# Kernel tuning notes

Hardware: AMD Instinct MI355X
Metric: run time of the kernel (lower is better)

## Reference

```python
import jax, jax.numpy as jnp
import numpy as np

NUM_HEADS = 16
NUM_KV_HEADS = 8
HEAD_DIM = 128
SCALE = 1.0 / np.sqrt(HEAD_DIM)  # 0.08838834764831845
SEQ_LENS = [1536, 512, 1024, 1024]  # ragged packed sequences, total T=4096


def setup_inputs() -> dict:
    key = jax.random.key(0)
    k1, k2, k3 = jax.random.split(key, 3)
    T = sum(SEQ_LENS)
    q = jax.random.normal(k1, (T, NUM_HEADS * HEAD_DIM), dtype=jnp.float32)
    k = jax.random.normal(k2, (T, NUM_KV_HEADS * HEAD_DIM), dtype=jnp.float32)
    v = jax.random.normal(k3, (T, NUM_KV_HEADS * HEAD_DIM), dtype=jnp.float32)
    # positions restart at 0 for each packed sequence; jumps mark boundaries
    positions = jnp.asarray(np.concatenate([np.arange(L) for L in SEQ_LENS]), dtype=jnp.int32)
    return {"q": q, "k": k, "v": v, "positions": positions}


def reference(q, k, v, positions):
    T = q.shape[0]
    G = NUM_HEADS // NUM_KV_HEADS  # GQA group size
    qh = q.reshape(T, NUM_KV_HEADS, G, HEAD_DIM)
    kh = k.reshape(T, NUM_KV_HEADS, HEAD_DIM)
    vh = v.reshape(T, NUM_KV_HEADS, HEAD_DIM)
    # segment ids from position jumps (positions[i] != positions[i-1] + 1)
    jump = jnp.concatenate([
        jnp.zeros((1,), jnp.int32),
        (positions[1:] != positions[:-1] + 1).astype(jnp.int32),
    ])
    seg = jnp.cumsum(jump)  # [T]
    idx = jnp.arange(T)
    # attend only within the same packed sequence, causally
    mask = (seg[:, None] == seg[None, :]) & (idx[:, None] >= idx[None, :])  # [T, T]
    # scores: [kv_head, group, T_q, T_k]
    scores = jnp.einsum('tkgd,skd->kgts', qh, kh) * jnp.float32(SCALE)
    scores = jnp.where(mask[None, None], scores, jnp.float32(-1e30))
    p = jax.nn.softmax(scores, axis=-1)
    o = jnp.einsum('kgts,skd->tkgd', p, vh)
    return o.reshape(T, NUM_HEADS * HEAD_DIM)
```

## Files before the change

kernel.cpp:

```cpp
#include <hip/hip_runtime.h>
#include <cstdint>
#include <cstddef>

#define NUM_KV   8
#define GQA      2
#define HD       128
#define QSTRIDE  2048
#define KSTRIDE  1024
#define SCALE_LOG2E 0.12751741032075463f

typedef float    f32x4  __attribute__((ext_vector_type(4)));
typedef float    f32x2  __attribute__((ext_vector_type(2)));
typedef float    f32x16 __attribute__((ext_vector_type(16)));
typedef unsigned u32x4  __attribute__((ext_vector_type(4)));
typedef __bf16   bf16x8 __attribute__((ext_vector_type(8)));
typedef __bf16   bf16x2 __attribute__((ext_vector_type(2)));
typedef int      i32x2  __attribute__((ext_vector_type(2)));

union U8 { unsigned short u[8]; unsigned d[4]; u32x4 q; bf16x8 v; };

__device__ __forceinline__ unsigned pkb(float x, float y) {
    f32x2 f = {x, y};
    bf16x2 b = __builtin_convertvector(f, bf16x2);
    union { bf16x2 b; unsigned u; } c; c.b = b;
    return c.u;
}

__device__ __forceinline__ void pl32swap(unsigned &a, unsigned &b) {
    i32x2 r = __builtin_amdgcn_permlane32_swap((int)a, (int)b, false, false);
    a = (unsigned)r[0];
    b = (unsigned)r[1];
}

__global__ __launch_bounds__(512)
void swizzle_kv(const float* __restrict__ kg, const float* __restrict__ vg,
                unsigned short* __restrict__ Kswz, unsigned short* __restrict__ Vswz,
                int T, int NT)
{
    const int tt = blockIdx.x, h = blockIdx.y;
    const int tid = threadIdx.x;
    const int f = tid >> 6, lane = tid & 63;
    const int col = lane & 31, hk = lane >> 5;

    if (blockIdx.z == 0) {
        const int row = min(tt * 32 + col, T - 1);
        const float* src = kg + (size_t)row * KSTRIDE + h * HD + f * 16 + hk * 8;
        f32x4 a = ((const f32x4*)src)[0];
        f32x4 b = ((const f32x4*)src)[1];
        u32x4 W;
        W[0] = pkb(a[0], a[1]); W[1] = pkb(a[2], a[3]);
        W[2] = pkb(b[0], b[1]); W[3] = pkb(b[2], b[3]);
        *(u32x4*)(Kswz + (((size_t)h * NT + tt) * 8 + f) * 512 + lane * 8) = W;
    } else {
        const int d  = (f >> 1) * 32 + col;
        const int r0 = tt * 32 + (f & 1) * 16 + hk * 8;
        float x[8];
#pragma unroll
        for (int j = 0; j < 8; ++j) {
            const int row = min(r0 + j, T - 1);
            x[j] = vg[(size_t)row * KSTRIDE + h * HD + d];
        }
        u32x4 W;
        W[0] = pkb(x[0], x[1]); W[1] = pkb(x[2], x[3]);
        W[2] = pkb(x[4], x[5]); W[3] = pkb(x[6], x[7]);
        *(u32x4*)(Vswz + (((size_t)h * NT + tt) * 8 + f) * 512 + lane * 8) = W;
    }
}

__global__ __launch_bounds__(128, 2)
void attn_kernel(const float* __restrict__ qg, const unsigned short* __restrict__ Kswz,
                 const unsigned short* __restrict__ Vswz, const int* __restrict__ pos,
                 float* __restrict__ out, int T, int NT)
{
    __shared__ __align__(16) float Xb[64 * 64 + 32];
    __shared__ int Db[256];
    __shared__ int Sq[256];

    const int tid  = threadIdx.x;
    const int w    = tid >> 6;
    const int lane = tid & 63;
    const int col  = lane & 31;
    const int hk   = lane >> 5;

    const int bid = blockIdx.x;
    const int kvh = bid & 7;
    const int g   = (bid >> 3) & 1;
    const int qtr = bid >> 4;
    const int nq  = (T + 31) >> 5;

    for (int t = tid; t < nq; t += 128) {
        const int r0  = t * 32;
        const int tlo = (r0 - pos[r0]) >> 5;
        const int thi = (min(r0 + 32, T) + 31) >> 5;
        Db[t] = thi - tlo;
    }
    __syncthreads();
    for (int t = tid; t < nq; t += 128) {
        const int dt = Db[t];
        int rk = 0;
        for (int j = 0; j < nq; ++j) {
            const int dj = Db[j];
            rk += (dj > dt) || (dj == dt && j < t);
        }
        Sq[rk] = t;
    }
    __syncthreads();

    const int qt   = Sq[qtr];
    const int row0 = qt * 32;
    const int hq   = kvh * GQA + g;

    const int kend = min(row0 + 32, T);
    const int k_lo = row0 - pos[row0];

    const int qrow   = min(row0 + col, T - 1);
    const int rstart = qrow - pos[qrow];
    int rs_max = rstart;
    rs_max = max(rs_max, __shfl_xor(rs_max, 1));
    rs_max = max(rs_max, __shfl_xor(rs_max, 2));
    rs_max = max(rs_max, __shfl_xor(rs_max, 4));
    rs_max = max(rs_max, __shfl_xor(rs_max, 8));
    rs_max = max(rs_max, __shfl_xor(rs_max, 16));

    bf16x8 qf[8];
    {
        const float* qp = qg + (size_t)qrow * QSTRIDE + hq * HD + hk * 8;
#pragma unroll
        for (int c = 0; c < 8; ++c) {
            f32x4 f0 = ((const f32x4*)(qp + c * 16))[0];
            f32x4 f1 = ((const f32x4*)(qp + c * 16))[1];
            U8 u;
            u.d[0] = pkb(f0[0] * SCALE_LOG2E, f0[1] * SCALE_LOG2E);
            u.d[1] = pkb(f0[2] * SCALE_LOG2E, f0[3] * SCALE_LOG2E);
            u.d[2] = pkb(f1[0] * SCALE_LOG2E, f1[1] * SCALE_LOG2E);
            u.d[3] = pkb(f1[2] * SCALE_LOG2E, f1[3] * SCALE_LOG2E);
            qf[c] = u.v;
        }
    }

    f32x16 acc[4];
#pragma unroll
    for (int nt = 0; nt < 4; ++nt)
#pragma unroll
        for (int r = 0; r < 16; ++r) acc[nt][r] = 0.f;
    float l_lane = 0.f;

    const int t_lo = k_lo >> 5;
    const int t_hi = (kend + 31) >> 5;
    const unsigned short* kb_base = Kswz + (size_t)kvh * NT * 4096;
    const unsigned short* vb_base = Vswz + (size_t)kvh * NT * 4096;

    U8 kf[8], kfn[8], vf[8];
    int tt = t_lo + w;
    if (tt < t_hi) {
        const unsigned short* kp = kb_base + (size_t)tt * 4096 + lane * 8;
#pragma unroll
        for (int c = 0; c < 8; ++c) kf[c].q = *(const u32x4*)(kp + c * 512);
    }

    for (; tt < t_hi; tt += 2) {
        {
            const unsigned short* vp = vb_base + (size_t)tt * 4096 + lane * 8;
#pragma unroll
            for (int f = 0; f < 8; ++f) vf[f].q = *(const u32x4*)(vp + f * 512);
        }
        const int ttn = tt + 2;
        if (ttn < t_hi) {
            const unsigned short* kp = kb_base + (size_t)ttn * 4096 + lane * 8;
#pragma unroll
            for (int c = 0; c < 8; ++c) kfn[c].q = *(const u32x4*)(kp + c * 512);
        }

        f32x16 s;
#pragma unroll
        for (int r = 0; r < 16; ++r) s[r] = 0.f;
        __builtin_amdgcn_s_setprio(1);
#pragma unroll
        for (int c = 0; c < 8; ++c)
            s = __builtin_amdgcn_mfma_f32_32x32x16_bf16(kf[c].v, qf[c], s, 0, 0, 0);
        __builtin_amdgcn_s_setprio(0);

        const int kb = tt * 32;
        float p[16];
        if (kb >= rs_max && kb + 32 <= row0 + 1) {
#pragma unroll
            for (int r = 0; r < 16; ++r) { p[r] = exp2f(s[r]); l_lane += p[r]; }
        } else {
#pragma unroll
            for (int r = 0; r < 16; ++r) {
                const int key = kb + (r & 3) + 8 * (r >> 2) + 4 * hk;
                const float x = (key >= rstart && key <= qrow) ? s[r] : -3e38f;
                p[r] = exp2f(x);
                l_lane += p[r];
            }
        }

        unsigned a0 = pkb(p[0],  p[1]),  a1 = pkb(p[2],  p[3]);
        unsigned b0 = pkb(p[4],  p[5]),  b1 = pkb(p[6],  p[7]);
        pl32swap(a0, b0); pl32swap(a1, b1);
        unsigned c0 = pkb(p[8],  p[9]),  c1 = pkb(p[10], p[11]);
        unsigned d0 = pkb(p[12], p[13]), d1 = pkb(p[14], p[15]);
        pl32swap(c0, d0); pl32swap(c1, d1);
        U8 pa0, pa1;
        pa0.d[0] = a0; pa0.d[1] = a1; pa0.d[2] = b0; pa0.d[3] = b1;
        pa1.d[0] = c0; pa1.d[1] = c1; pa1.d[2] = d0; pa1.d[3] = d1;

        __builtin_amdgcn_s_setprio(1);
#pragma unroll
        for (int nt = 0; nt < 4; ++nt) {
            acc[nt] = __builtin_amdgcn_mfma_f32_32x32x16_bf16(pa0.v, vf[nt * 2].v,     acc[nt], 0, 0, 0);
            acc[nt] = __builtin_amdgcn_mfma_f32_32x32x16_bf16(pa1.v, vf[nt * 2 + 1].v, acc[nt], 0, 0, 0);
        }
        __builtin_amdgcn_s_setprio(0);

#pragma unroll
        for (int c = 0; c < 8; ++c) kf[c] = kfn[c];
    }

    const float lt = l_lane + __shfl_xor(l_lane, 32);

    if (w == 1) {
#pragma unroll
        for (int nt = 0; nt < 4; ++nt)
#pragma unroll
            for (int r = 0; r < 16; ++r)
                Xb[(nt * 16 + r) * 64 + lane] = acc[nt][r];
        if (hk == 0) Xb[4096 + col] = lt;
    }
    __syncthreads();
    if (w == 0) {
        const float ltot = lt + Xb[4096 + col];
#pragma unroll
        for (int nt = 0; nt < 4; ++nt)
#pragma unroll
            for (int r = 0; r < 16; ++r)
                acc[nt][r] += Xb[(nt * 16 + r) * 64 + lane];

#pragma unroll
        for (int r = 0; r < 16; ++r) {
            const int m  = (r & 3) + 8 * (r >> 2) + 4 * hk;
            const int rg = row0 + m;
            const float lm  = __shfl(ltot, m);
            const float inv = (lm > 0.f) ? (1.0f / lm) : 0.f;
            if (rg < T) {
                float* op = out + (size_t)rg * QSTRIDE + hq * HD + col;
#pragma unroll
                for (int nt = 0; nt < 4; ++nt)
                    op[nt * 32] = acc[nt][r] * inv;
            }
        }
    }
}

extern "C" void kernel_launch(void* const* d_in, const int* in_sizes, int n_in,
                              void* d_out, int out_size, void* d_ws, size_t ws_size,
                              hipStream_t stream) {
    const float* q   = (const float*)d_in[0];
    const float* k   = (const float*)d_in[1];
    const float* v   = (const float*)d_in[2];
    const int*   pos = (const int*)d_in[3];
    float* out = (float*)d_out;
    const int T  = in_sizes[0] / QSTRIDE;
    const int NT = (T + 31) / 32;

    unsigned short* Kswz = (unsigned short*)d_ws;
    unsigned short* Vswz = Kswz + (size_t)NUM_KV * NT * 4096;

    swizzle_kv<<<dim3(NT, NUM_KV, 2), 512, 0, stream>>>(k, v, Kswz, Vswz, T, NT);
    attn_kernel<<<dim3(NT * 16), 128, 0, stream>>>(q, Kswz, Vswz, pos, out, T, NT);
}
```

Before: 149.8 us.

## Split KV tiles across four waves per query tile with tree reduction

Each block now runs four waves instead of two, with the waves striding over key/value tiles by four. The partial accumulators and row sums are combined through shared memory in two stages, a pairwise reduction followed by a final merge. The aim is to shorten the per-block serial loop over KV tiles for long sequences. The trade-off is higher register pressure under launch_bounds(256,1), fewer resident blocks per CU, and extra reduction traffic and barriers.

```diff
diff --git a/kernel.cpp b/kernel.cpp
--- a/kernel.cpp
+++ b/kernel.cpp
@@ -67,12 +67,12 @@
     }
 }
 
-__global__ __launch_bounds__(128, 2)
+__global__ __launch_bounds__(256, 1)
 void attn_kernel(const float* __restrict__ qg, const unsigned short* __restrict__ Kswz,
                  const unsigned short* __restrict__ Vswz, const int* __restrict__ pos,
                  float* __restrict__ out, int T, int NT)
 {
-    __shared__ __align__(16) float Xb[64 * 64 + 32];
+    __shared__ __align__(16) float Xb[2][4128];
     __shared__ int Db[256];
     __shared__ int Sq[256];
 
@@ -88,14 +88,14 @@
     const int qtr = bid >> 4;
     const int nq  = (T + 31) >> 5;
 
-    for (int t = tid; t < nq; t += 128) {
+    for (int t = tid; t < nq; t += 256) {
         const int r0  = t * 32;
         const int tlo = (r0 - pos[r0]) >> 5;
         const int thi = (min(r0 + 32, T) + 31) >> 5;
         Db[t] = thi - tlo;
     }
     __syncthreads();
-    for (int t = tid; t < nq; t += 128) {
+    for (int t = tid; t < nq; t += 256) {
         const int dt = Db[t];
         int rk = 0;
         for (int j = 0; j < nq; ++j) {
@@ -108,6 +108,7 @@
 
     const int qt   = Sq[qtr];
     const int row0 = qt * 32;
+    if (row0 >= T) return;
     const int hq   = kvh * GQA + g;
 
     const int kend = min(row0 + 32, T);
@@ -158,17 +159,17 @@
         for (int c = 0; c < 8; ++c) kf[c].q = *(const u32x4*)(kp + c * 512);
     }
 
-    for (; tt < t_hi; tt += 2) {
+    for (; tt < t_hi; tt += 4) {
+        const int ttn = tt + 4;
+        if (ttn < t_hi) {
+            const unsigned short* kp = kb_base + (size_t)ttn * 4096 + lane * 8;
+#pragma unroll
+            for (int c = 0; c < 8; ++c) kfn[c].q = *(const u32x4*)(kp + c * 512);
+        }
         {
             const unsigned short* vp = vb_base + (size_t)tt * 4096 + lane * 8;
 #pragma unroll
             for (int f = 0; f < 8; ++f) vf[f].q = *(const u32x4*)(vp + f * 512);
-        }
-        const int ttn = tt + 2;
-        if (ttn < t_hi) {
-            const unsigned short* kp = kb_base + (size_t)ttn * 4096 + lane * 8;
-#pragma unroll
-            for (int c = 0; c < 8; ++c) kfn[c].q = *(const u32x4*)(kp + c * 512);
         }
 
         f32x16 s;
@@ -217,24 +218,46 @@
         for (int c = 0; c < 8; ++c) kf[c] = kfn[c];
     }
 
-    const float lt = l_lane + __shfl_xor(l_lane, 32);
-
-    if (w == 1) {
-#pragma unroll
-        for (int nt = 0; nt < 4; ++nt)
-#pragma unroll
-            for (int r = 0; r < 16; ++r)
-                Xb[(nt * 16 + r) * 64 + lane] = acc[nt][r];
-        if (hk == 0) Xb[4096 + col] = lt;
+    float ltW = l_lane + __shfl_xor(l_lane, 32);
+
+    if (w & 1) {
+        float* B = Xb[w >> 1];
+#pragma unroll
+        for (int nt = 0; nt < 4; ++nt)
+#pragma unroll
+            for (int r = 0; r < 16; ++r)
+                B[(nt * 16 + r) * 64 + lane] = acc[nt][r];
+        if (hk == 0) B[4096 + col] = ltW;
+    }
+    __syncthreads();
+    if (!(w & 1)) {
+        const float* B = Xb[w >> 1];
+#pragma unroll
+        for (int nt = 0; nt < 4; ++nt)
+#pragma unroll
+            for (int r = 0; r < 16; ++r)
+                acc[nt][r] += B[(nt * 16 + r) * 64 + lane];
+        ltW += B[4096 + col];
+    }
+    __syncthreads();
+    if (w == 2) {
+        float* B = Xb[0];
+#pragma unroll
+        for (int nt = 0; nt < 4; ++nt)
+#pragma unroll
+            for (int r = 0; r < 16; ++r)
+                B[(nt * 16 + r) * 64 + lane] = acc[nt][r];
+        if (hk == 0) B[4096 + col] = ltW;
     }
     __syncthreads();
     if (w == 0) {
-        const float ltot = lt + Xb[4096 + col];
-#pragma unroll
-        for (int nt = 0; nt < 4; ++nt)
-#pragma unroll
-            for (int r = 0; r < 16; ++r)
-                acc[nt][r] += Xb[(nt * 16 + r) * 64 + lane];
+        const float* B = Xb[0];
+        const float ltot = ltW + B[4096 + col];
+#pragma unroll
+        for (int nt = 0; nt < 4; ++nt)
+#pragma unroll
+            for (int r = 0; r < 16; ++r)
+                acc[nt][r] += B[(nt * 16 + r) * 64 + lane];
 
 #pragma unroll
         for (int r = 0; r < 16; ++r) {
@@ -267,5 +290,5 @@
     unsigned short* Vswz = Kswz + (size_t)NUM_KV * NT * 4096;
 
     swizzle_kv<<<dim3(NT, NUM_KV, 2), 512, 0, stream>>>(k, v, Kswz, Vswz, T, NT);
-    attn_kernel<<<dim3(NT * 16), 128, 0, stream>>>(q, Kswz, Vswz, pos, out, T, NT);
-}
+    attn_kernel<<<dim3(NT * 16), 256, 0, stream>>>(q, Kswz, Vswz, pos, out, T, NT);
+}
```

Measured after the change: 168.6 us. +12.6%, slower.
